# Kernel optimization log

Hardware: AMD Instinct MI355X
Metric: run time of the kernel (lower is better)

The kernel has to match this reference:

```python
import jax, jax.numpy as jnp
import numpy as np

# Instant-NGP style multi-resolution hash grid (torch-ngp convention)
NUM_LEVELS = 32
LEVEL_DIM = 2
LOG2_T = 19
T = 1 << LOG2_T            # per-level hash table size (power of two)
BASE_RES = 1
PER_LEVEL_SCALE = 2.0
PRIMES = (1, 2654435761, 805459861)  # spatial hash primes (uint32, wraps)
# 8 corner offsets of the unit cube, [8, 3]
OFFSETS_NP = np.array([[(c >> d) & 1 for d in range(3)] for c in range(8)], dtype=np.uint32)


def hash_encode(x, embeddings):
    """x: [N,3] in [0,1); embeddings: [L, T, F] -> [N, L*F]."""
    offsets = jnp.asarray(OFFSETS_NP)                       # [8,3] uint32
    offs_f = offsets.astype(x.dtype)                        # [8,3]
    feats = []
    for l in range(NUM_LEVELS):
        scale = float(np.exp2(l * np.log2(PER_LEVEL_SCALE)) * BASE_RES - 1.0)
        res = int(np.ceil(scale)) + 1
        pos = x * jnp.float32(scale) + 0.5                  # [N,3]
        pos0 = jnp.floor(pos)
        frac = pos - pos0                                   # [N,3] in [0,1)
        pg = pos0.astype(jnp.uint32)                        # [N,3]
        corners = pg[:, None, :] + offsets[None, :, :]      # [N,8,3] uint32
        if res ** 3 <= T:
            # dense (non-colliding) linear index at coarse levels
            r = jnp.uint32(res)
            idx = corners[..., 0] + corners[..., 1] * r + corners[..., 2] * (r * r)
        else:
            # spatial hash: xor of coordinate * prime (uint32 wraparound)
            idx = (corners[..., 0] * jnp.uint32(PRIMES[0])
                   ^ corners[..., 1] * jnp.uint32(PRIMES[1])
                   ^ corners[..., 2] * jnp.uint32(PRIMES[2]))
        idx = (idx & jnp.uint32(T - 1)).astype(jnp.int32)   # [N,8]
        f = embeddings[l][idx]                              # gather -> [N,8,F]
        # trilinear interpolation weights
        w = jnp.prod(jnp.where(offs_f[None] == 1, frac[:, None, :], 1.0 - frac[:, None, :]), axis=-1)  # [N,8]
        feats.append(jnp.sum(f * w[..., None], axis=1))     # [N,F]
    return jnp.concatenate(feats, axis=-1)                  # [N, L*F]


def setup_inputs() -> dict:
    key = jax.random.key(0)
    k = jax.random.split(key, 5)
    N = 1 << 20
    x = jax.random.uniform(k[0], (N, 3), dtype=jnp.float32)
    embeddings = jax.random.normal(k[1], (NUM_LEVELS, T, LEVEL_DIM), dtype=jnp.float32) * 1e-2
    in_dim = NUM_LEVELS * LEVEL_DIM  # 64
    W1 = jax.random.normal(k[2], (in_dim, 128), dtype=jnp.float32) * (1.0 / np.sqrt(in_dim))
    b1 = jnp.zeros((128,), jnp.float32)
    W2 = jax.random.normal(k[3], (128, 128), dtype=jnp.float32) * (1.0 / np.sqrt(128))
    b2 = jnp.zeros((128,), jnp.float32)
    W3 = jax.random.normal(k[4], (128, 1), dtype=jnp.float32) * (1.0 / np.sqrt(128))
    b3 = jnp.zeros((1,), jnp.float32)
    return {"x": x, "embeddings": embeddings, "W1": W1, "b1": b1, "W2": W2, "b2": b2, "W3": W3, "b3": b3}


def reference(x, embeddings, W1, b1, W2, b2, W3, b3):
    h = hash_encode(x, embeddings)                 # [N, 64]
    h = jax.nn.relu(h @ W1 + b1)                   # [N, 128]
    h = jax.nn.relu(h @ W2 + b2)                   # [N, 128]
    return h @ W3 + b3                             # [N, 1]
```

## Files before the change

### kernel.cpp

```cpp
#include <hip/hip_runtime.h>
#include <stdint.h>


#define NLV 32
#define LOG2T 19
#define TSZ (1u << LOG2T)
#define TMASK (TSZ - 1u)
#define PRIME2 2654435761u
#define PRIME3 805459861u

typedef float v2f __attribute__((ext_vector_type(2)));
typedef float f32x4 __attribute__((ext_vector_type(4)));
typedef float f32x4u __attribute__((ext_vector_type(4), aligned(8)));
typedef short bf16x8 __attribute__((ext_vector_type(8)));
typedef uint32_t u32x4 __attribute__((ext_vector_type(4)));

__device__ __forceinline__ uint32_t pack_bf16(float a, float b) {
  uint32_t ua = __float_as_uint(a), ub = __float_as_uint(b);
  ua = (ua + 0x7fffu + ((ua >> 16) & 1u)) >> 16;
  ub = (ub + 0x7fffu + ((ub >> 16) & 1u)) >> 16;
  return ua | (ub << 16);
}
__device__ __forceinline__ uint16_t bf16_rne(float a) {
  uint32_t u = __float_as_uint(a);
  u = (u + 0x7fffu + ((u >> 16) & 1u)) >> 16;
  return (uint16_t)u;
}

__global__ __launch_bounds__(256) void encode_kernel(
    const float* __restrict__ x, const float* __restrict__ emb,
    uint32_t* __restrict__ feats, int offset, int count, int chunkCap, int bpl)
{
  const int bid = (int)blockIdx.x;
  const int xcd = bid & 7;
  const int j = bid >> 3;
  const int phase = j / bpl;
  const int within = j - phase * bpl;
  const int l = xcd + (phase << 3);

  const float scale = (float)((double)(1ULL << l) - 1.0);
  const uint32_t r = 1u << l, rr = r * r;
  const bool dense = (l <= 6);
  const v2f* __restrict__ embl = (const v2f*)(emb + ((size_t)l << (LOG2T + 1)));

  #pragma unroll
  for (int k = 0; k < 4; ++k) {
    int li = within * 1024 + k * 256 + (int)threadIdx.x;
    if (li < count) {
      int p = offset + li;
      float xv = __builtin_nontemporal_load(&x[3 * p + 0]);
      float yv = __builtin_nontemporal_load(&x[3 * p + 1]);
      float zv = __builtin_nontemporal_load(&x[3 * p + 2]);
      float px = __fadd_rn(__fmul_rn(xv, scale), 0.5f);
      float py = __fadd_rn(__fmul_rn(yv, scale), 0.5f);
      float pz = __fadd_rn(__fmul_rn(zv, scale), 0.5f);
      float bx = floorf(px), by = floorf(py), bz = floorf(pz);
      float fx = __fsub_rn(px, bx), fy = __fsub_rn(py, by), fz = __fsub_rn(pz, bz);
      uint32_t gx = (uint32_t)bx, gy = (uint32_t)by, gz = (uint32_t)bz;
      float wx0 = __fsub_rn(1.0f, fx), wx1 = fx;
      float wy0 = __fsub_rn(1.0f, fy), wy1 = fy;
      float wz0 = __fsub_rn(1.0f, fz), wz1 = fz;

      float f0 = 0.0f, f1 = 0.0f;
      #pragma unroll
      for (int cp = 0; cp < 4; ++cp) {
        uint32_t cy = gy + (uint32_t)(cp & 1);
        uint32_t cz = gz + (uint32_t)(cp >> 1);
        float wyz = __fmul_rn((cp & 1) ? wy1 : wy0, (cp >> 1) ? wz1 : wz0);
        v2f e0, e1;
        if (dense) {
          uint32_t i0 = gx + cy * r + cz * rr;
          f32x4 e2 = *(const f32x4u*)&embl[i0];
          e0[0] = e2.x; e0[1] = e2.y; e1[0] = e2.z; e1[1] = e2.w;
        } else {
          uint32_t h = (cy * PRIME2) ^ (cz * PRIME3);
          uint32_t i0 = (gx ^ h) & TMASK;
          if (!(gx & 1u)) {
            f32x4 e2 = *(const f32x4*)&embl[i0 & ~1u];
            bool odd = (i0 & 1u) != 0u;
            e0[0] = odd ? e2.z : e2.x; e0[1] = odd ? e2.w : e2.y;
            e1[0] = odd ? e2.x : e2.z; e1[1] = odd ? e2.y : e2.w;
          } else {
            uint32_t i1 = ((gx + 1u) ^ h) & TMASK;
            e0 = embl[i0];
            e1 = embl[i1];
          }
        }
        float w0 = __fmul_rn(wx0, wyz), w1 = __fmul_rn(wx1, wyz);
        f0 = fmaf(w0, e0[0], f0); f1 = fmaf(w0, e0[1], f1);
        f0 = fmaf(w1, e1[0], f0); f1 = fmaf(w1, e1[1], f1);
      }
      __builtin_nontemporal_store(pack_bf16(f0, f1),
                                  &feats[(size_t)l * (size_t)chunkCap + li]);
    }
  }
}

__global__ __launch_bounds__(512) void prep_kernel(
    const float* __restrict__ W1, const float* __restrict__ W2,
    uint16_t* __restrict__ wimg)
{
  int i = (int)blockIdx.x * 512 + (int)threadIdx.x;
  if (i < 8192) {
    int k = i >> 7, n = i & 127;
    wimg[(n * 128 + ((k * 2) ^ ((n & 7) << 4))) >> 1] = bf16_rne(W1[i]);
  } else if (i < 24576) {
    int t = i - 8192;
    int k = t >> 7, n = t & 127;
    wimg[(16384 + n * 256 + ((k * 2) ^ ((n & 7) << 4))) >> 1] = bf16_rne(W2[t]);
  }
}

#define MLP_G 64

__global__ __launch_bounds__(256, 2) void mlp_kernel(
    const uint32_t* __restrict__ feats, const uint16_t* __restrict__ wimg,
    const float* __restrict__ b1, const float* __restrict__ b2,
    const float* __restrict__ W3, const float* __restrict__ b3,
    float* __restrict__ out, int offset, int count, int chunkCap, int nGroups)
{
  __shared__ char lds[65536];
  char* xh  = lds;
  char* wt1 = lds + 16384;
  char* wb  = lds + 32768;

  const int tid = (int)threadIdx.x;
  const int lane = tid & 63;
  const int w = tid >> 6;
  const int col = lane & 15;
  const int kh = lane >> 4;

  #pragma unroll
  for (int jj = 0; jj < 12; ++jj) {
    int i = tid + jj * 256;
    ((u32x4*)wt1)[i] = ((const u32x4*)wimg)[i];
  }

  const int p = w * 16 + col;
  float bias1[8], bias2[8], w3v[8];
  #pragma unroll
  for (int nt = 0; nt < 8; ++nt) {
    int n = nt * 16 + col;
    bias1[nt] = b1[n]; bias2[nt] = b2[n]; w3v[nt] = W3[n];
  }
  const float b3v = b3[0];

  for (int g = (int)blockIdx.x; g < nGroups; g += (int)gridDim.x) {
    const int base = g * MLP_G;
    __syncthreads();

    {
      int pp = tid & 63, q = tid >> 6;
      int gp = base + pp;
      int src = (gp < count) ? gp : 0;
      #pragma unroll
      for (int s = 0; s < 2; ++s) {
        int pl = q * 8 + s * 4;
        u32x4 v;
        v.x = __builtin_nontemporal_load(&feats[(size_t)(pl + 0) * chunkCap + src]);
        v.y = __builtin_nontemporal_load(&feats[(size_t)(pl + 1) * chunkCap + src]);
        v.z = __builtin_nontemporal_load(&feats[(size_t)(pl + 2) * chunkCap + src]);
        v.w = __builtin_nontemporal_load(&feats[(size_t)(pl + 3) * chunkCap + src]);
        *(u32x4*)(xh + pp * 256 + ((pl * 4) ^ ((pp & 7) << 4))) = v;
      }
    }
    __syncthreads();

    f32x4 acc[8];
    #pragma unroll
    for (int nt = 0; nt < 8; ++nt) acc[nt] = {0.f, 0.f, 0.f, 0.f};
    #pragma unroll
    for (int kt = 0; kt < 2; ++kt) {
      bf16x8 a = *(const bf16x8*)(xh + p * 256 + ((kt * 64 + kh * 16) ^ ((p & 7) << 4)));
      #pragma unroll
      for (int nt = 0; nt < 8; ++nt) {
        int n = nt * 16 + col;
        bf16x8 b = *(const bf16x8*)(wt1 + n * 128 + ((kt * 64 + kh * 16) ^ ((n & 7) << 4)));
        acc[nt] = __builtin_amdgcn_mfma_f32_16x16x32_bf16(a, b, acc[nt], 0, 0, 0);
      }
    }
    __syncthreads();

    #pragma unroll
    for (int nt = 0; nt < 8; ++nt) {
      int n = nt * 16 + col;
      #pragma unroll
      for (int rg = 0; rg < 4; ++rg) {
        int pr = w * 16 + kh * 4 + rg;
        float h = fmaxf(acc[nt][rg] + bias1[nt], 0.0f);
        *(uint16_t*)(xh + pr * 256 + ((n * 2) ^ ((pr & 7) << 4))) = bf16_rne(h);
      }
    }
    __syncthreads();

    f32x4 acc2[8];
    #pragma unroll
    for (int nt = 0; nt < 8; ++nt) acc2[nt] = {0.f, 0.f, 0.f, 0.f};
    #pragma unroll
    for (int q = 0; q < 4; ++q) {
      bf16x8 a = *(const bf16x8*)(xh + p * 256 + ((q * 64 + kh * 16) ^ ((p & 7) << 4)));
      #pragma unroll
      for (int nt = 0; nt < 8; ++nt) {
        int n = nt * 16 + col;
        bf16x8 b = *(const bf16x8*)(wb + n * 256 + ((q * 64 + kh * 16) ^ ((n & 7) << 4)));
        acc2[nt] = __builtin_amdgcn_mfma_f32_16x16x32_bf16(a, b, acc2[nt], 0, 0, 0);
      }
    }

    float osum[4] = {0.f, 0.f, 0.f, 0.f};
    #pragma unroll
    for (int nt = 0; nt < 8; ++nt) {
      #pragma unroll
      for (int rg = 0; rg < 4; ++rg)
        osum[rg] = fmaf(fmaxf(acc2[nt][rg] + bias2[nt], 0.0f), w3v[nt], osum[rg]);
    }
    #pragma unroll
    for (int rg = 0; rg < 4; ++rg) {
      osum[rg] += __shfl_xor(osum[rg], 1);
      osum[rg] += __shfl_xor(osum[rg], 2);
      osum[rg] += __shfl_xor(osum[rg], 4);
      osum[rg] += __shfl_xor(osum[rg], 8);
    }
    #pragma unroll
    for (int rg = 0; rg < 4; ++rg) {
      if (col == rg) {
        int pr = base + w * 16 + kh * 4 + rg;
        if (pr < count) out[offset + pr] = osum[rg] + b3v;
      }
    }
  }
}

extern "C" void kernel_launch(void* const* d_in, const int* in_sizes, int n_in,
                              void* d_out, int out_size, void* d_ws, size_t ws_size,
                              hipStream_t stream) {
  const float* x   = (const float*)d_in[0];
  const float* emb = (const float*)d_in[1];
  const float* W1  = (const float*)d_in[2];
  const float* b1  = (const float*)d_in[3];
  const float* W2  = (const float*)d_in[4];
  const float* b2  = (const float*)d_in[5];
  const float* W3  = (const float*)d_in[6];
  const float* b3  = (const float*)d_in[7];
  float* out = (float*)d_out;
  const int N = in_sizes[0] / 3;

  uint16_t* wimg = (uint16_t*)d_ws;
  uint32_t* feats = (uint32_t*)((char*)d_ws + 49152);
  const size_t perPoint = (size_t)NLV * sizeof(uint32_t);
  size_t avail = (ws_size > 49152) ? ws_size - 49152 : 0;
  size_t capz = avail / perPoint;
  if (capz > (size_t)N) capz = (size_t)N;
  int cap = (int)capz & ~1023;
  if (cap <= 0) cap = (N < 1024) ? N : 1024;

  prep_kernel<<<48, 512, 0, stream>>>(W1, W2, wimg);

  for (int off = 0; off < N; off += cap) {
    int cnt = (N - off < cap) ? (N - off) : cap;
    int bpl = (cnt + 1023) / 1024;
    encode_kernel<<<32 * bpl, 256, 0, stream>>>(x, emb, feats, off, cnt, cap, bpl);
    int nGroups = (cnt + MLP_G - 1) / MLP_G;
    int nb = nGroups < 2048 ? nGroups : 2048;
    mlp_kernel<<<nb, 256, 0, stream>>>(
        feats, wimg, b1, b2, W3, b3, out, off, cnt, cap, nGroups);
  }
}
```

Measured before the change: 1.010 ms.

## Keep MLP weights in registers, prefetch next group's features, swap GEMM1 operands

The MLP kernel now loads the W1 and W2 bf16 fragments into registers once, instead of staging them in LDS and re-reading them every group. It prefetches the next group's features into registers while the current group computes. GEMM1 swaps its operands so the hidden activations come out transposed and can be packed and written to LDS as bf16 pairs, which removes one barrier. This cuts LDS traffic and hides global load latency, but register pressure grows a lot and occupancy falls to one block per SIMD set (launch bounds 256,1).

Result: slower. 1.056 ms (+4.5%).

```diff
diff --git a/kernel.cpp b/kernel.cpp
--- a/kernel.cpp
+++ b/kernel.cpp
@@ -14,6 +14,7 @@
 typedef float f32x4u __attribute__((ext_vector_type(4), aligned(8)));
 typedef short bf16x8 __attribute__((ext_vector_type(8)));
 typedef uint32_t u32x4 __attribute__((ext_vector_type(4)));
+typedef uint32_t u32x2 __attribute__((ext_vector_type(2)));
 
 __device__ __forceinline__ uint32_t pack_bf16(float a, float b) {
   uint32_t ua = __float_as_uint(a), ub = __float_as_uint(b);
@@ -113,98 +114,125 @@
 
 #define MLP_G 64
 
-__global__ __launch_bounds__(256, 2) void mlp_kernel(
+__global__ __launch_bounds__(256, 1) void mlp_kernel(
     const uint32_t* __restrict__ feats, const uint16_t* __restrict__ wimg,
     const float* __restrict__ b1, const float* __restrict__ b2,
     const float* __restrict__ W3, const float* __restrict__ b3,
     float* __restrict__ out, int offset, int count, int chunkCap, int nGroups)
 {
-  __shared__ char lds[65536];
-  char* xh  = lds;
-  char* wt1 = lds + 16384;
-  char* wb  = lds + 32768;
+  __shared__ char lds[24576];
+  char* xb = lds;
+  char* hb = lds + 8192;
 
   const int tid = (int)threadIdx.x;
   const int lane = tid & 63;
   const int w = tid >> 6;
   const int col = lane & 15;
   const int kh = lane >> 4;
-
-  #pragma unroll
-  for (int jj = 0; jj < 12; ++jj) {
-    int i = tid + jj * 256;
-    ((u32x4*)wt1)[i] = ((const u32x4*)wimg)[i];
-  }
-
-  const int p = w * 16 + col;
-  float bias1[8], bias2[8], w3v[8];
+  const char* wbytes = (const char*)wimg;
+
+  bf16x8 w1f[2][8], w2f[4][8];
   #pragma unroll
   for (int nt = 0; nt < 8; ++nt) {
     int n = nt * 16 + col;
-    bias1[nt] = b1[n]; bias2[nt] = b2[n]; w3v[nt] = W3[n];
+    #pragma unroll
+    for (int kt = 0; kt < 2; ++kt)
+      w1f[kt][nt] = *(const bf16x8*)(wbytes + n * 128 +
+                        ((kt * 64 + kh * 16) ^ ((n & 7) << 4)));
+    #pragma unroll
+    for (int q = 0; q < 4; ++q)
+      w2f[q][nt] = *(const bf16x8*)(wbytes + 16384 + n * 256 +
+                        ((q * 64 + kh * 16) ^ ((n & 7) << 4)));
+  }
+  float bias1r[8][4];
+  #pragma unroll
+  for (int nt = 0; nt < 8; ++nt)
+    #pragma unroll
+    for (int rg = 0; rg < 4; ++rg)
+      bias1r[nt][rg] = b1[nt * 16 + kh * 4 + rg];
+  float bias2[8], w3v[8];
+  #pragma unroll
+  for (int nt = 0; nt < 8; ++nt) {
+    bias2[nt] = b2[nt * 16 + col];
+    w3v[nt] = W3[nt * 16 + col];
   }
   const float b3v = b3[0];
 
-  for (int g = (int)blockIdx.x; g < nGroups; g += (int)gridDim.x) {
-    const int base = g * MLP_G;
+  const int pp = w * 16 + col;
+  const int sp = tid & 63;
+  const int sq = tid >> 6;
+
+  int g = (int)blockIdx.x;
+  u32x4 xr0, xr1;
+  {
+    int src = g * MLP_G + sp; if (src >= count) src = 0;
+    int pl = sq * 8;
+    xr0.x = __builtin_nontemporal_load(&feats[(size_t)(pl + 0) * chunkCap + src]);
+    xr0.y = __builtin_nontemporal_load(&feats[(size_t)(pl + 1) * chunkCap + src]);
+    xr0.z = __builtin_nontemporal_load(&feats[(size_t)(pl + 2) * chunkCap + src]);
+    xr0.w = __builtin_nontemporal_load(&feats[(size_t)(pl + 3) * chunkCap + src]);
+    xr1.x = __builtin_nontemporal_load(&feats[(size_t)(pl + 4) * chunkCap + src]);
+    xr1.y = __builtin_nontemporal_load(&feats[(size_t)(pl + 5) * chunkCap + src]);
+    xr1.z = __builtin_nontemporal_load(&feats[(size_t)(pl + 6) * chunkCap + src]);
+    xr1.w = __builtin_nontemporal_load(&feats[(size_t)(pl + 7) * chunkCap + src]);
+  }
+
+  for (; g < nGroups; g += (int)gridDim.x) {
+    *(u32x4*)(xb + sp * 128 + ((sq * 32 +  0) ^ ((sp & 7) << 4))) = xr0;
+    *(u32x4*)(xb + sp * 128 + ((sq * 32 + 16) ^ ((sp & 7) << 4))) = xr1;
     __syncthreads();
 
     {
-      int pp = tid & 63, q = tid >> 6;
-      int gp = base + pp;
-      int src = (gp < count) ? gp : 0;
-      #pragma unroll
-      for (int s = 0; s < 2; ++s) {
-        int pl = q * 8 + s * 4;
-        u32x4 v;
-        v.x = __builtin_nontemporal_load(&feats[(size_t)(pl + 0) * chunkCap + src]);
-        v.y = __builtin_nontemporal_load(&feats[(size_t)(pl + 1) * chunkCap + src]);
-        v.z = __builtin_nontemporal_load(&feats[(size_t)(pl + 2) * chunkCap + src]);
-        v.w = __builtin_nontemporal_load(&feats[(size_t)(pl + 3) * chunkCap + src]);
-        *(u32x4*)(xh + pp * 256 + ((pl * 4) ^ ((pp & 7) << 4))) = v;
-      }
+      int gn = g + (int)gridDim.x; if (gn >= nGroups) gn = g;
+      int src = gn * MLP_G + sp; if (src >= count) src = 0;
+      int pl = sq * 8;
+      xr0.x = __builtin_nontemporal_load(&feats[(size_t)(pl + 0) * chunkCap + src]);
+      xr0.y = __builtin_nontemporal_load(&feats[(size_t)(pl + 1) * chunkCap + src]);
+      xr0.z = __builtin_nontemporal_load(&feats[(size_t)(pl + 2) * chunkCap + src]);
+      xr0.w = __builtin_nontemporal_load(&feats[(size_t)(pl + 3) * chunkCap + src]);
+      xr1.x = __builtin_nontemporal_load(&feats[(size_t)(pl + 4) * chunkCap + src]);
+      xr1.y = __builtin_nontemporal_load(&feats[(size_t)(pl + 5) * chunkCap + src]);
+      xr1.z = __builtin_nontemporal_load(&feats[(size_t)(pl + 6) * chunkCap + src]);
+      xr1.w = __builtin_nontemporal_load(&feats[(size_t)(pl + 7) * chunkCap + src]);
+    }
+
+    bf16x8 xa[2];
+    #pragma unroll
+    for (int kt = 0; kt < 2; ++kt)
+      xa[kt] = *(const bf16x8*)(xb + pp * 128 +
+                   ((kt * 64 + kh * 16) ^ ((pp & 7) << 4)));
+    f32x4 acc[8];
+    #pragma unroll
+    for (int nt = 0; nt < 8; ++nt) acc[nt] = {0.f, 0.f, 0.f, 0.f};
+    #pragma unroll
+    for (int kt = 0; kt < 2; ++kt)
+      #pragma unroll
+      for (int nt = 0; nt < 8; ++nt)
+        acc[nt] = __builtin_amdgcn_mfma_f32_16x16x32_bf16(
+                      w1f[kt][nt], xa[kt], acc[nt], 0, 0, 0);
+
+    #pragma unroll
+    for (int nt = 0; nt < 8; ++nt) {
+      uint32_t lo = pack_bf16(fmaxf(acc[nt][0] + bias1r[nt][0], 0.0f),
+                              fmaxf(acc[nt][1] + bias1r[nt][1], 0.0f));
+      uint32_t hi = pack_bf16(fmaxf(acc[nt][2] + bias1r[nt][2], 0.0f),
+                              fmaxf(acc[nt][3] + bias1r[nt][3], 0.0f));
+      u32x2 v; v.x = lo; v.y = hi;
+      *(u32x2*)(hb + pp * 256 + ((nt * 32 + kh * 8) ^ ((pp & 7) << 4))) = v;
     }
     __syncthreads();
 
-    f32x4 acc[8];
-    #pragma unroll
-    for (int nt = 0; nt < 8; ++nt) acc[nt] = {0.f, 0.f, 0.f, 0.f};
-    #pragma unroll
-    for (int kt = 0; kt < 2; ++kt) {
-      bf16x8 a = *(const bf16x8*)(xh + p * 256 + ((kt * 64 + kh * 16) ^ ((p & 7) << 4)));
-      #pragma unroll
-      for (int nt = 0; nt < 8; ++nt) {
-        int n = nt * 16 + col;
-        bf16x8 b = *(const bf16x8*)(wt1 + n * 128 + ((kt * 64 + kh * 16) ^ ((n & 7) << 4)));
-        acc[nt] = __builtin_amdgcn_mfma_f32_16x16x32_bf16(a, b, acc[nt], 0, 0, 0);
-      }
-    }
-    __syncthreads();
-
-    #pragma unroll
-    for (int nt = 0; nt < 8; ++nt) {
-      int n = nt * 16 + col;
-      #pragma unroll
-      for (int rg = 0; rg < 4; ++rg) {
-        int pr = w * 16 + kh * 4 + rg;
-        float h = fmaxf(acc[nt][rg] + bias1[nt], 0.0f);
-        *(uint16_t*)(xh + pr * 256 + ((n * 2) ^ ((pr & 7) << 4))) = bf16_rne(h);
-      }
-    }
-    __syncthreads();
-
     f32x4 acc2[8];
     #pragma unroll
     for (int nt = 0; nt < 8; ++nt) acc2[nt] = {0.f, 0.f, 0.f, 0.f};
     #pragma unroll
     for (int q = 0; q < 4; ++q) {
-      bf16x8 a = *(const bf16x8*)(xh + p * 256 + ((q * 64 + kh * 16) ^ ((p & 7) << 4)));
-      #pragma unroll
-      for (int nt = 0; nt < 8; ++nt) {
-        int n = nt * 16 + col;
-        bf16x8 b = *(const bf16x8*)(wb + n * 256 + ((q * 64 + kh * 16) ^ ((n & 7) << 4)));
-        acc2[nt] = __builtin_amdgcn_mfma_f32_16x16x32_bf16(a, b, acc2[nt], 0, 0, 0);
-      }
+      bf16x8 ha = *(const bf16x8*)(hb + pp * 256 +
+                      ((q * 64 + kh * 16) ^ ((pp & 7) << 4)));
+      #pragma unroll
+      for (int nt = 0; nt < 8; ++nt)
+        acc2[nt] = __builtin_amdgcn_mfma_f32_16x16x32_bf16(
+                       ha, w2f[q][nt], acc2[nt], 0, 0, 0);
     }
 
     float osum[4] = {0.f, 0.f, 0.f, 0.f};
@@ -221,6 +249,7 @@
       osum[rg] += __shfl_xor(osum[rg], 4);
       osum[rg] += __shfl_xor(osum[rg], 8);
     }
+    const int base = g * MLP_G;
     #pragma unroll
     for (int rg = 0; rg < 4; ++rg) {
       if (col == rg) {
```

## Fuse dense coarse levels and last hash level into MLP kernel

Applied to the files above, without the earlier changes.

The encode kernel now handles only the 24 hashed levels 7–30, and the feature buffer shrinks from 32 to 24 entries per point. The MLP kernel's LDS staging computes the dense levels 0–6 (in wave 0) and level 31 (in wave 3) directly from x and the embeddings. This cuts intermediate feature write and read traffic and keeps the encode grid a multiple of the 8-way XCD mapping. Two block-wide barriers between the MLP layers are also dropped, since each wave only reads and writes its own rows. The cost is uneven work across waves during staging and extra register pressure in the MLP kernel.

Result: faster. 937.3 us (-7.2%).

```diff
diff --git a/kernel.cpp b/kernel.cpp
--- a/kernel.cpp
+++ b/kernel.cpp
@@ -8,6 +8,7 @@
 #define TMASK (TSZ - 1u)
 #define PRIME2 2654435761u
 #define PRIME3 805459861u
+#define NHASH 24
 
 typedef float v2f __attribute__((ext_vector_type(2)));
 typedef float f32x4 __attribute__((ext_vector_type(4)));
@@ -25,6 +26,53 @@
   uint32_t u = __float_as_uint(a);
   u = (u + 0x7fffu + ((u >> 16) & 1u)) >> 16;
   return (uint16_t)u;
+}
+
+__device__ __forceinline__ uint32_t encode_level(
+    float scale, uint32_t r, bool dense, const v2f* __restrict__ embl,
+    float xv, float yv, float zv)
+{
+  float px = __fadd_rn(__fmul_rn(xv, scale), 0.5f);
+  float py = __fadd_rn(__fmul_rn(yv, scale), 0.5f);
+  float pz = __fadd_rn(__fmul_rn(zv, scale), 0.5f);
+  float bx = floorf(px), by = floorf(py), bz = floorf(pz);
+  float fx = __fsub_rn(px, bx), fy = __fsub_rn(py, by), fz = __fsub_rn(pz, bz);
+  uint32_t gx = (uint32_t)bx, gy = (uint32_t)by, gz = (uint32_t)bz;
+  float wx0 = __fsub_rn(1.0f, fx), wx1 = fx;
+  float wy0 = __fsub_rn(1.0f, fy), wy1 = fy;
+  float wz0 = __fsub_rn(1.0f, fz), wz1 = fz;
+  const uint32_t rr = r * r;
+
+  float f0 = 0.0f, f1 = 0.0f;
+  #pragma unroll
+  for (int cp = 0; cp < 4; ++cp) {
+    uint32_t cy = gy + (uint32_t)(cp & 1);
+    uint32_t cz = gz + (uint32_t)(cp >> 1);
+    float wyz = __fmul_rn((cp & 1) ? wy1 : wy0, (cp >> 1) ? wz1 : wz0);
+    v2f e0, e1;
+    if (dense) {
+      uint32_t i0 = gx + cy * r + cz * rr;
+      f32x4 e2 = *(const f32x4u*)&embl[i0];
+      e0[0] = e2.x; e0[1] = e2.y; e1[0] = e2.z; e1[1] = e2.w;
+    } else {
+      uint32_t h = (cy * PRIME2) ^ (cz * PRIME3);
+      uint32_t i0 = (gx ^ h) & TMASK;
+      if (!(gx & 1u)) {
+        f32x4 e2 = *(const f32x4*)&embl[i0 & ~1u];
+        bool odd = (i0 & 1u) != 0u;
+        e0[0] = odd ? e2.z : e2.x; e0[1] = odd ? e2.w : e2.y;
+        e1[0] = odd ? e2.x : e2.z; e1[1] = odd ? e2.y : e2.w;
+      } else {
+        uint32_t i1 = ((gx + 1u) ^ h) & TMASK;
+        e0 = embl[i0];
+        e1 = embl[i1];
+      }
+    }
+    float w0 = __fmul_rn(wx0, wyz), w1 = __fmul_rn(wx1, wyz);
+    f0 = fmaf(w0, e0[0], f0); f1 = fmaf(w0, e0[1], f1);
+    f0 = fmaf(w1, e1[0], f0); f1 = fmaf(w1, e1[1], f1);
+  }
+  return pack_bf16(f0, f1);
 }
 
 __global__ __launch_bounds__(256) void encode_kernel(
@@ -36,11 +84,9 @@
   const int j = bid >> 3;
   const int phase = j / bpl;
   const int within = j - phase * bpl;
-  const int l = xcd + (phase << 3);
+  const int l = 7 + xcd + (phase << 3);
 
   const float scale = (float)((double)(1ULL << l) - 1.0);
-  const uint32_t r = 1u << l, rr = r * r;
-  const bool dense = (l <= 6);
   const v2f* __restrict__ embl = (const v2f*)(emb + ((size_t)l << (LOG2T + 1)));
 
   #pragma unroll
@@ -51,47 +97,8 @@
       float xv = __builtin_nontemporal_load(&x[3 * p + 0]);
       float yv = __builtin_nontemporal_load(&x[3 * p + 1]);
       float zv = __builtin_nontemporal_load(&x[3 * p + 2]);
-      float px = __fadd_rn(__fmul_rn(xv, scale), 0.5f);
-      float py = __fadd_rn(__fmul_rn(yv, scale), 0.5f);
-      float pz = __fadd_rn(__fmul_rn(zv, scale), 0.5f);
-      float bx = floorf(px), by = floorf(py), bz = floorf(pz);
-      float fx = __fsub_rn(px, bx), fy = __fsub_rn(py, by), fz = __fsub_rn(pz, bz);
-      uint32_t gx = (uint32_t)bx, gy = (uint32_t)by, gz = (uint32_t)bz;
-      float wx0 = __fsub_rn(1.0f, fx), wx1 = fx;
-      float wy0 = __fsub_rn(1.0f, fy), wy1 = fy;
-      float wz0 = __fsub_rn(1.0f, fz), wz1 = fz;
-
-      float f0 = 0.0f, f1 = 0.0f;
-      #pragma unroll
-      for (int cp = 0; cp < 4; ++cp) {
-        uint32_t cy = gy + (uint32_t)(cp & 1);
-        uint32_t cz = gz + (uint32_t)(cp >> 1);
-        float wyz = __fmul_rn((cp & 1) ? wy1 : wy0, (cp >> 1) ? wz1 : wz0);
-        v2f e0, e1;
-        if (dense) {
-          uint32_t i0 = gx + cy * r + cz * rr;
-          f32x4 e2 = *(const f32x4u*)&embl[i0];
-          e0[0] = e2.x; e0[1] = e2.y; e1[0] = e2.z; e1[1] = e2.w;
-        } else {
-          uint32_t h = (cy * PRIME2) ^ (cz * PRIME3);
-          uint32_t i0 = (gx ^ h) & TMASK;
-          if (!(gx & 1u)) {
-            f32x4 e2 = *(const f32x4*)&embl[i0 & ~1u];
-            bool odd = (i0 & 1u) != 0u;
-            e0[0] = odd ? e2.z : e2.x; e0[1] = odd ? e2.w : e2.y;
-            e1[0] = odd ? e2.x : e2.z; e1[1] = odd ? e2.y : e2.w;
-          } else {
-            uint32_t i1 = ((gx + 1u) ^ h) & TMASK;
-            e0 = embl[i0];
-            e1 = embl[i1];
-          }
-        }
-        float w0 = __fmul_rn(wx0, wyz), w1 = __fmul_rn(wx1, wyz);
-        f0 = fmaf(w0, e0[0], f0); f1 = fmaf(w0, e0[1], f1);
-        f0 = fmaf(w1, e1[0], f0); f1 = fmaf(w1, e1[1], f1);
-      }
-      __builtin_nontemporal_store(pack_bf16(f0, f1),
-                                  &feats[(size_t)l * (size_t)chunkCap + li]);
+      uint32_t f = encode_level(scale, 0u, false, embl, xv, yv, zv);
+      __builtin_nontemporal_store(f, &feats[(size_t)(l - 7) * chunkCap + li]);
     }
   }
 }
@@ -114,6 +121,7 @@
 #define MLP_G 64
 
 __global__ __launch_bounds__(256, 2) void mlp_kernel(
+    const float* __restrict__ x, const float* __restrict__ emb,
     const uint32_t* __restrict__ feats, const uint16_t* __restrict__ wimg,
     const float* __restrict__ b1, const float* __restrict__ b2,
     const float* __restrict__ W3, const float* __restrict__ b3,
@@ -136,7 +144,7 @@
     ((u32x4*)wt1)[i] = ((const u32x4*)wimg)[i];
   }
 
-  const int p = w * 16 + col;
+  const int pp = w * 16 + col;
   float bias1[8], bias2[8], w3v[8];
   #pragma unroll
   for (int nt = 0; nt < 8; ++nt) {
@@ -145,24 +153,55 @@
   }
   const float b3v = b3[0];
 
+  const int sp = tid & 63;
+  const int sq = tid >> 6;
+
   for (int g = (int)blockIdx.x; g < nGroups; g += (int)gridDim.x) {
     const int base = g * MLP_G;
     __syncthreads();
 
     {
-      int pp = tid & 63, q = tid >> 6;
-      int gp = base + pp;
+      int gp = base + sp;
       int src = (gp < count) ? gp : 0;
-      #pragma unroll
-      for (int s = 0; s < 2; ++s) {
-        int pl = q * 8 + s * 4;
-        u32x4 v;
-        v.x = __builtin_nontemporal_load(&feats[(size_t)(pl + 0) * chunkCap + src]);
-        v.y = __builtin_nontemporal_load(&feats[(size_t)(pl + 1) * chunkCap + src]);
-        v.z = __builtin_nontemporal_load(&feats[(size_t)(pl + 2) * chunkCap + src]);
-        v.w = __builtin_nontemporal_load(&feats[(size_t)(pl + 3) * chunkCap + src]);
-        *(u32x4*)(xh + pp * 256 + ((pl * 4) ^ ((pp & 7) << 4))) = v;
-      }
+      u32x4 v0, v1;
+      if (sq == 0) {
+        float xv = x[3 * src + 0], yv = x[3 * src + 1], zv = x[3 * src + 2];
+        uint32_t f[7];
+        #pragma unroll
+        for (int l = 0; l < 7; ++l) {
+          const float scale = (float)((double)(1ULL << l) - 1.0);
+          const v2f* embl = (const v2f*)(emb + ((size_t)l << (LOG2T + 1)));
+          f[l] = encode_level(scale, 1u << l, true, embl, xv, yv, zv);
+        }
+        v0.x = f[0]; v0.y = f[1]; v0.z = f[2]; v0.w = f[3];
+        v1.x = f[4]; v1.y = f[5]; v1.z = f[6];
+        v1.w = __builtin_nontemporal_load(&feats[(size_t)0 * chunkCap + src]);
+      } else if (sq == 3) {
+        float xv = x[3 * src + 0], yv = x[3 * src + 1], zv = x[3 * src + 2];
+        v0.x = __builtin_nontemporal_load(&feats[(size_t)17 * chunkCap + src]);
+        v0.y = __builtin_nontemporal_load(&feats[(size_t)18 * chunkCap + src]);
+        v0.z = __builtin_nontemporal_load(&feats[(size_t)19 * chunkCap + src]);
+        v0.w = __builtin_nontemporal_load(&feats[(size_t)20 * chunkCap + src]);
+        v1.x = __builtin_nontemporal_load(&feats[(size_t)21 * chunkCap + src]);
+        v1.y = __builtin_nontemporal_load(&feats[(size_t)22 * chunkCap + src]);
+        v1.z = __builtin_nontemporal_load(&feats[(size_t)23 * chunkCap + src]);
+        const float s31 = (float)((double)(1ULL << 31) - 1.0);
+        const v2f* embl = (const v2f*)(emb + ((size_t)31 << (LOG2T + 1)));
+        v1.w = encode_level(s31, 0u, false, embl, xv, yv, zv);
+      } else {
+        int ib = sq * 8 - 7;
+        v0.x = __builtin_nontemporal_load(&feats[(size_t)(ib + 0) * chunkCap + src]);
+        v0.y = __builtin_nontemporal_load(&feats[(size_t)(ib + 1) * chunkCap + src]);
+        v0.z = __builtin_nontemporal_load(&feats[(size_t)(ib + 2) * chunkCap + src]);
+        v0.w = __builtin_nontemporal_load(&feats[(size_t)(ib + 3) * chunkCap + src]);
+        v1.x = __builtin_nontemporal_load(&feats[(size_t)(ib + 4) * chunkCap + src]);
+        v1.y = __builtin_nontemporal_load(&feats[(size_t)(ib + 5) * chunkCap + src]);
+        v1.z = __builtin_nontemporal_load(&feats[(size_t)(ib + 6) * chunkCap + src]);
+        v1.w = __builtin_nontemporal_load(&feats[(size_t)(ib + 7) * chunkCap + src]);
+      }
+      int sw = (sp & 7) << 4;
+      *(u32x4*)(xh + sp * 256 + ((sq * 32 +  0) ^ sw)) = v0;
+      *(u32x4*)(xh + sp * 256 + ((sq * 32 + 16) ^ sw)) = v1;
     }
     __syncthreads();
 
@@ -171,7 +210,7 @@
     for (int nt = 0; nt < 8; ++nt) acc[nt] = {0.f, 0.f, 0.f, 0.f};
     #pragma unroll
     for (int kt = 0; kt < 2; ++kt) {
-      bf16x8 a = *(const bf16x8*)(xh + p * 256 + ((kt * 64 + kh * 16) ^ ((p & 7) << 4)));
+      bf16x8 a = *(const bf16x8*)(xh + pp * 256 + ((kt * 64 + kh * 16) ^ ((pp & 7) << 4)));
       #pragma unroll
       for (int nt = 0; nt < 8; ++nt) {
         int n = nt * 16 + col;
@@ -179,7 +218,6 @@
         acc[nt] = __builtin_amdgcn_mfma_f32_16x16x32_bf16(a, b, acc[nt], 0, 0, 0);
       }
     }
-    __syncthreads();
 
     #pragma unroll
     for (int nt = 0; nt < 8; ++nt) {
@@ -191,14 +229,13 @@
         *(uint16_t*)(xh + pr * 256 + ((n * 2) ^ ((pr & 7) << 4))) = bf16_rne(h);
       }
     }
-    __syncthreads();
 
     f32x4 acc2[8];
     #pragma unroll
     for (int nt = 0; nt < 8; ++nt) acc2[nt] = {0.f, 0.f, 0.f, 0.f};
     #pragma unroll
     for (int q = 0; q < 4; ++q) {
-      bf16x8 a = *(const bf16x8*)(xh + p * 256 + ((q * 64 + kh * 16) ^ ((p & 7) << 4)));
+      bf16x8 a = *(const bf16x8*)(xh + pp * 256 + ((q * 64 + kh * 16) ^ ((pp & 7) << 4)));
       #pragma unroll
       for (int nt = 0; nt < 8; ++nt) {
         int n = nt * 16 + col;
@@ -247,7 +284,7 @@
 
   uint16_t* wimg = (uint16_t*)d_ws;
   uint32_t* feats = (uint32_t*)((char*)d_ws + 49152);
-  const size_t perPoint = (size_t)NLV * sizeof(uint32_t);
+  const size_t perPoint = (size_t)NHASH * sizeof(uint32_t);
   size_t avail = (ws_size > 49152) ? ws_size - 49152 : 0;
   size_t capz = avail / perPoint;
   if (capz > (size_t)N) capz = (size_t)N;
@@ -259,10 +296,10 @@
   for (int off = 0; off < N; off += cap) {
     int cnt = (N - off < cap) ? (N - off) : cap;
     int bpl = (cnt + 1023) / 1024;
-    encode_kernel<<<32 * bpl, 256, 0, stream>>>(x, emb, feats, off, cnt, cap, bpl);
+    encode_kernel<<<NHASH * bpl, 256, 0, stream>>>(x, emb, feats, off, cnt, cap, bpl);
     int nGroups = (cnt + MLP_G - 1) / MLP_G;
     int nb = nGroups < 2048 ? nGroups : 2048;
     mlp_kernel<<<nb, 256, 0, stream>>>(
-        feats, wimg, b1, b2, W3, b3, out, off, cnt, cap, nGroups);
-  }
-}
+        x, emb, feats, wimg, b1, b2, W3, b3, out, off, cnt, cap, nGroups);
+  }
+}
```
